# Performance work log

Measured on AMD Instinct MI355X. Metric: run time of the kernel, lower is better.

Reference implementation:

```python
import jax, jax.numpy as jnp
import numpy as np

N, S, F, D = 4096, 128, 128, 256  # batch, memory slots, feat_dim, dim_h_o
EPS = 1e-8  # torch CosineSimilarity eps


def _xavier(key, shape):
    fan_out, fan_in = shape
    std = float(np.sqrt(2.0 / (fan_in + fan_out)))
    return jax.random.normal(key, shape, dtype=jnp.float32) * std


def setup_inputs() -> dict:
    key = jax.random.key(0)
    ks = jax.random.split(key, 10)
    return {
        "h_o_prev": jax.random.normal(ks[0], (N, D), dtype=jnp.float32),
        "C": jax.random.normal(ks[1], (N, S, F), dtype=jnp.float32),
        "Wk": _xavier(ks[2], (F, D)), "bk": jnp.zeros((F,), jnp.float32),
        "Wb": _xavier(ks[3], (1, D)), "bb": jnp.zeros((1,), jnp.float32),
        "We": _xavier(ks[4], (F, D)), "be": jnp.zeros((F,), jnp.float32),
        "Wv": _xavier(ks[5], (F, D)), "bv": jnp.zeros((F,), jnp.float32),
        "Wih": _xavier(ks[6], (3 * D, F)), "Whh": _xavier(ks[7], (3 * D, D)),
        "bih": jnp.zeros((3 * D,), jnp.float32), "bhh": jnp.zeros((3 * D,), jnp.float32),
    }


def reference(h_o_prev, C, Wk, bk, Wb, bb, We, be, Wv, bv, Wih, Whh, bih, bhh):
    # --- Attention (content addressing) ---
    k = h_o_prev @ Wk.T + bk                              # [N, F]
    beta_pre = h_o_prev @ Wb.T + bb                       # [N, 1]
    # clamp-split softplus trick in source == softplus(x) + 1
    beta = jax.nn.softplus(beta_pre) + 1.0                # [N, 1]
    C_norm = jnp.maximum(jnp.linalg.norm(C, axis=2), EPS)           # [N, S]
    k_norm = jnp.maximum(jnp.linalg.norm(k, axis=1, keepdims=True), EPS)  # [N, 1]
    s = jnp.einsum("nsf,nf->ns", C, k) / (C_norm * k_norm)          # cosine sim [N, S]
    w = jax.nn.softmax(s * beta, axis=1)                  # [N, S]
    # --- Read memory ---
    r = jnp.einsum("ns,nsf->nf", w, C)                    # [N, F]
    # --- GRU cell update (torch GRUCell semantics) ---
    gi = r @ Wih.T + bih                                  # [N, 3D]
    gh = h_o_prev @ Whh.T + bhh                           # [N, 3D]
    i_r, i_z, i_n = jnp.split(gi, 3, axis=1)
    h_r, h_z, h_n = jnp.split(gh, 3, axis=1)
    rg = jax.nn.sigmoid(i_r + h_r)
    z = jax.nn.sigmoid(i_z + h_z)
    n = jnp.tanh(i_n + rg * h_n)
    h_o = (1.0 - z) * n + z * h_o_prev                    # [N, D]
    # --- Write memory (erase + add, outer products) ---
    e = jax.nn.sigmoid(h_o @ We.T + be)                   # [N, F]
    v = h_o @ Wv.T + bv                                   # [N, F]
    w2 = w[:, :, None]                                    # [N, S, 1]
    C_new = C * (1.0 - w2 * e[:, None, :]) + w2 * v[:, None, :]
    return h_o, C_new, k, r
```

## Files before the change

### kernel.cpp

```cpp
#include <hip/hip_runtime.h>
#include <hip/hip_bf16.h>
#include <cstddef>
#include <cstdint>

constexpr int Nn = 4096;
constexpr int Ss = 128;
constexpr int Ff = 128;
constexpr int Dd = 256;
constexpr float EPSV = 1e-8f;

constexpr size_t HO_OFF = 0;
constexpr size_t C_OFF  = (size_t)Nn * Dd;
constexpr size_t K_OFF  = C_OFF + (size_t)Nn * Ss * Ff;
constexpr size_t R_OFF  = K_OFF + (size_t)Nn * Ff;

typedef __attribute__((ext_vector_type(4))) float f4v;
typedef __attribute__((ext_vector_type(8))) short bh8;
typedef __attribute__((ext_vector_type(4))) short bh4;

constexpr int WK_O  = 0;
constexpr int WHH_O = 32768;
constexpr int WIH_O = 229376;
constexpr int WEV_O = 327680;
constexpr int W_TOT = 393216;

__device__ __forceinline__ float sigmf(float x) { return 1.0f / (1.0f + __expf(-x)); }

__device__ __forceinline__ short f2bf(float x) {
    __hip_bfloat16 h = __float2bfloat16(x);
    return *reinterpret_cast<short*>(&h);
}

__device__ __forceinline__ int swzH(int row, int kb) { return row * 512 + (kb ^ ((row & 7) << 4)); }
__device__ __forceinline__ int swzR(int row, int kb) { return row * 256 + (kb ^ ((row & 7) << 4)); }

__device__ __forceinline__ f4v mfma16(bh8 a, bh8 b, f4v c) {
    return __builtin_amdgcn_mfma_f32_16x16x32_bf16(a, b, c, 0, 0, 0);
}

__global__ __launch_bounds__(256) void prep_weights(
    const float* __restrict__ Wk, const float* __restrict__ Whh,
    const float* __restrict__ Wih, const float* __restrict__ We,
    const float* __restrict__ Wv, short* __restrict__ out)
{
    int id = blockIdx.x * 256 + threadIdx.x;
    float v;
    if      (id < WHH_O) v = Wk[id - WK_O];
    else if (id < WIH_O) v = Whh[id - WHH_O];
    else if (id < WEV_O) v = Wih[id - WIH_O];
    else if (id < WEV_O + 32768) v = We[id - WEV_O];
    else v = Wv[id - WEV_O - 32768];
    out[id] = f2bf(v);
}

__global__ __launch_bounds__(512, 4) void mega_kernel(
    const float* __restrict__ C, const float* __restrict__ h_prev,
    const short* __restrict__ WB,
    const float* __restrict__ Wb, const float* __restrict__ bb,
    const float* __restrict__ bk, const float* __restrict__ bhh,
    const float* __restrict__ bih, const float* __restrict__ be,
    const float* __restrict__ bv,
    float* __restrict__ ho, float* __restrict__ Cnew,
    float* __restrict__ kout, float* __restrict__ rout)
{
    __shared__ float sH[8][256];
    __shared__ __align__(16) short sHb[16 * 256];
    __shared__ __align__(16) short sRb[16 * 128];
    __shared__ float sK[8][128];
    __shared__ float sSc[8][128];
    __shared__ float sGs[8][768];
    __shared__ float sGn[8][256];
    __shared__ float sEV[8][256];

    const int t  = threadIdx.x;
    const int l  = t & 63;
    const int wv = t >> 6;
    const int nb = blockIdx.x * 8;
    char* hb = (char*)sHb;
    char* rb = (char*)sRb;

    const short* WkB  = WB + WK_O;
    const short* WhhB = WB + WHH_O;
    const short* WihB = WB + WIH_O;
    const short* WevB = WB + WEV_O;

    {
        const int f = t * 4, row = f >> 8, col = f & 255;
        float4 hv = *(const float4*)(h_prev + (size_t)(nb + row) * Dd + col);
        *(float4*)&sH[row][col] = hv;
        bh4 hb4 = { f2bf(hv.x), f2bf(hv.y), f2bf(hv.z), f2bf(hv.w) };
        *(bh4*)(hb + swzH(row, col * 2)) = hb4;
        *(int4*)(hb + 8192 + t * 16) = int4{0, 0, 0, 0};
        *(int*)(rb + 2048 + t * 4) = 0;
    }
    __syncthreads();

    {
        const int fr = l & 15, kq = l >> 4, rbase = kq * 4;
        const int colg = wv * 16 + fr;
        f4v acc = {0.f, 0.f, 0.f, 0.f};
#pragma unroll
        for (int kc = 0; kc < 8; ++kc) {
            bh8 a = *(const bh8*)(hb + swzH(fr, kc * 64 + kq * 16));
            bh8 b = *(const bh8*)(WkB + (size_t)colg * 256 + kc * 32 + kq * 8);
            acc = mfma16(a, b, acc);
        }
        if (rbase < 8) {
            const float bs = bk[colg];
#pragma unroll
            for (int rg = 0; rg < 4; ++rg) {
                float x = acc[rg] + bs;
                sK[rbase + rg][colg] = x;
                kout[(size_t)(nb + rbase + rg) * Ff + colg] = x;
            }
        }
    }
    __syncthreads();

    float M_r = 0.0f, invL_r = 0.0f;
    {
        const int half = l >> 5, fl = l & 31, f4 = fl * 4;
        const float* Cn = C + (size_t)(nb + wv) * (Ss * Ff);

        float kv0 = sK[wv][l], kv1 = sK[wv][64 + l];
        float ks = kv0 * kv0 + kv1 * kv1;
#pragma unroll
        for (int o = 32; o > 0; o >>= 1) ks += __shfl_xor(ks, o);
        const float knorm = fmaxf(sqrtf(ks), EPSV);

        float4 hv = *(const float4*)&sH[wv][l * 4];
        float4 wb4 = *(const float4*)(Wb + l * 4);
        float bp = hv.x * wb4.x + hv.y * wb4.y + hv.z * wb4.z + hv.w * wb4.w;
#pragma unroll
        for (int o = 32; o > 0; o >>= 1) bp += __shfl_xor(bp, o);
        bp += bb[0];
        const float beta = ((bp > 20.0f) ? bp : log1pf(__expf(bp))) + 1.0f;

        const float4 kreg = *(const float4*)&sK[wv][f4];
        float m = -INFINITY, lsum = 0.0f;
        f4v racc = {0.f, 0.f, 0.f, 0.f};
#pragma unroll 4
        for (int it = 0; it < 64; ++it) {
            const int s = it * 2 + half;
            f4v c4 = *(const f4v*)(Cn + s * Ff + f4);
            float d = c4.x * kreg.x + c4.y * kreg.y + c4.z * kreg.z + c4.w * kreg.w;
            float q = c4.x * c4.x + c4.y * c4.y + c4.z * c4.z + c4.w * c4.w;
#pragma unroll
            for (int o = 16; o > 0; o >>= 1) { d += __shfl_xor(d, o); q += __shfl_xor(q, o); }
            const float x = d / (fmaxf(sqrtf(q), EPSV) * knorm) * beta;
            if (fl == 0) sSc[wv][s] = x;
            const float mn   = fmaxf(m, x);
            const float corr = __expf(m - mn);
            const float p    = __expf(x - mn);
            lsum = lsum * corr + p;
            racc = racc * corr + p * c4;
            m = mn;
        }
        float m2 = __shfl_xor(m, 32);
        float l2 = __shfl_xor(lsum, 32);
        f4v r2;
        r2.x = __shfl_xor(racc.x, 32); r2.y = __shfl_xor(racc.y, 32);
        r2.z = __shfl_xor(racc.z, 32); r2.w = __shfl_xor(racc.w, 32);
        const float M  = fmaxf(m, m2);
        const float e1 = __expf(m - M), e2 = __expf(m2 - M);
        const float L  = lsum * e1 + l2 * e2;
        const float iL = 1.0f / L;
        f4v r4 = (racc * e1 + r2 * e2) * iL;
        if (half == 0) {
            *(f4v*)(rout + (size_t)(nb + wv) * Ff + f4) = r4;
            bh4 rb4 = { f2bf(r4.x), f2bf(r4.y), f2bf(r4.z), f2bf(r4.w) };
            *(bh4*)(rb + swzR(wv, f4 * 2)) = rb4;
        }
        M_r = M; invL_r = iL;
    }
    __syncthreads();

    {
        const int fr = l & 15, kq = l >> 4, rbase = kq * 4;
#pragma unroll
        for (int i = 0; i < 6; ++i) {
            const int colg = i * 128 + wv * 16 + fr;
            f4v aG = {0.f, 0.f, 0.f, 0.f}, aI = {0.f, 0.f, 0.f, 0.f};
#pragma unroll
            for (int kc = 0; kc < 8; ++kc) {
                bh8 a = *(const bh8*)(hb + swzH(fr, kc * 64 + kq * 16));
                bh8 b = *(const bh8*)(WhhB + (size_t)colg * 256 + kc * 32 + kq * 8);
                aG = mfma16(a, b, aG);
            }
#pragma unroll
            for (int kc = 0; kc < 4; ++kc) {
                bh8 a = *(const bh8*)(rb + swzR(fr, kc * 64 + kq * 16));
                bh8 b = *(const bh8*)(WihB + (size_t)colg * 128 + kc * 32 + kq * 8);
                aI = mfma16(a, b, aI);
            }
            if (rbase < 8) {
                if (colg < 512) {
                    const float bs = bhh[colg] + bih[colg];
#pragma unroll
                    for (int rg = 0; rg < 4; ++rg)
                        sGs[rbase + rg][colg] = aG[rg] + aI[rg] + bs;
                } else {
                    const float b1 = bhh[colg], b2 = bih[colg];
#pragma unroll
                    for (int rg = 0; rg < 4; ++rg) {
                        sGs[rbase + rg][colg]       = aG[rg] + b1;
                        sGn[rbase + rg][colg - 512] = aI[rg] + b2;
                    }
                }
            }
        }
    }
    __syncthreads();

    {
        const int d4 = l * 4;
        float4 gr  = *(const float4*)&sGs[wv][d4];
        float4 gz  = *(const float4*)&sGs[wv][256 + d4];
        float4 hn  = *(const float4*)&sGs[wv][512 + d4];
        float4 in_ = *(const float4*)&sGn[wv][d4];
        float4 hp  = *(const float4*)&sH[wv][d4];
        float4 o;
        { float rg = sigmf(gr.x), z = sigmf(gz.x);
          float nn = tanhf(in_.x + rg * hn.x); o.x = (1.0f - z) * nn + z * hp.x; }
        { float rg = sigmf(gr.y), z = sigmf(gz.y);
          float nn = tanhf(in_.y + rg * hn.y); o.y = (1.0f - z) * nn + z * hp.y; }
        { float rg = sigmf(gr.z), z = sigmf(gz.z);
          float nn = tanhf(in_.z + rg * hn.z); o.z = (1.0f - z) * nn + z * hp.z; }
        { float rg = sigmf(gr.w), z = sigmf(gz.w);
          float nn = tanhf(in_.w + rg * hn.w); o.w = (1.0f - z) * nn + z * hp.w; }
        *(float4*)(ho + (size_t)(nb + wv) * Dd + d4) = o;
        bh4 ob = { f2bf(o.x), f2bf(o.y), f2bf(o.z), f2bf(o.w) };
        *(bh4*)(hb + swzH(wv, d4 * 2)) = ob;
    }
    __syncthreads();

    {
        const int fr = l & 15, kq = l >> 4, rbase = kq * 4;
#pragma unroll
        for (int i = 0; i < 2; ++i) {
            const int colg = i * 128 + wv * 16 + fr;
            f4v acc = {0.f, 0.f, 0.f, 0.f};
#pragma unroll
            for (int kc = 0; kc < 8; ++kc) {
                bh8 a = *(const bh8*)(hb + swzH(fr, kc * 64 + kq * 16));
                bh8 b = *(const bh8*)(WevB + (size_t)colg * 256 + kc * 32 + kq * 8);
                acc = mfma16(a, b, acc);
            }
            if (rbase < 8) {
                const float bs = (colg < 128) ? be[colg] : bv[colg - 128];
#pragma unroll
                for (int rg = 0; rg < 4; ++rg) {
                    float x = acc[rg] + bs;
                    if (colg < 128) x = sigmf(x);
                    sEV[rbase + rg][colg] = x;
                }
            }
        }
    }
    __syncthreads();

    {
        const int half = l >> 5, fl = l & 31, f4 = fl * 4;
        const float* Cn = C    + (size_t)(nb + wv) * (Ss * Ff);
        float*       Co = Cnew + (size_t)(nb + wv) * (Ss * Ff);
        f4v e4 = *(const f4v*)&sEV[wv][f4];
        f4v v4 = *(const f4v*)&sEV[wv][128 + f4];
#pragma unroll 4
        for (int it = 0; it < 64; ++it) {
            const int s = it * 2 + half;
            const float wsc = __expf(sSc[wv][s] - M_r) * invL_r;
            f4v c4 = *(const f4v*)(Cn + s * Ff + f4);
            f4v o = c4 * (1.0f - wsc * e4) + wsc * v4;
            __builtin_nontemporal_store(o, (f4v*)(Co + s * Ff + f4));
        }
    }
}

extern "C" void kernel_launch(void* const* d_in, const int* in_sizes, int n_in,
                              void* d_out, int out_size, void* d_ws, size_t ws_size,
                              hipStream_t stream)
{
    const float* h_prev = (const float*)d_in[0];
    const float* C      = (const float*)d_in[1];
    const float* Wk     = (const float*)d_in[2];
    const float* bk     = (const float*)d_in[3];
    const float* Wb     = (const float*)d_in[4];
    const float* bb     = (const float*)d_in[5];
    const float* We     = (const float*)d_in[6];
    const float* be     = (const float*)d_in[7];
    const float* Wv     = (const float*)d_in[8];
    const float* bv     = (const float*)d_in[9];
    const float* Wih    = (const float*)d_in[10];
    const float* Whh    = (const float*)d_in[11];
    const float* bih    = (const float*)d_in[12];
    const float* bhh    = (const float*)d_in[13];

    float* out  = (float*)d_out;
    float* ho   = out + HO_OFF;
    float* Cnew = out + C_OFF;
    float* kbuf = out + K_OFF;
    float* rbuf = out + R_OFF;

    short* wsB = (short*)d_ws;

    prep_weights<<<W_TOT / 256, 256, 0, stream>>>(Wk, Whh, Wih, We, Wv, wsB);

    mega_kernel<<<Nn / 8, 512, 0, stream>>>(
        C, h_prev, wsB, Wb, bb, bk, bhh, bih, be, bv,
        ho, Cnew, kbuf, rbuf);
}
```

Before: 191.0 us.

## Prefetch C rows in register batches and use fixed-max softmax

Result: slower. 204.5 us (+7.1%).

```diff
diff --git a/kernel.cpp b/kernel.cpp
--- a/kernel.cpp
+++ b/kernel.cpp
@@ -117,7 +117,7 @@
     }
     __syncthreads();
 
-    float M_r = 0.0f, invL_r = 0.0f;
+    float invL_r = 0.0f;
     {
         const int half = l >> 5, fl = l & 31, f4 = fl * 4;
         const float* Cn = C + (size_t)(nb + wv) * (Ss * Ff);
@@ -137,41 +137,55 @@
         const float beta = ((bp > 20.0f) ? bp : log1pf(__expf(bp))) + 1.0f;
 
         const float4 kreg = *(const float4*)&sK[wv][f4];
-        float m = -INFINITY, lsum = 0.0f;
+        float lsum = 0.0f;
         f4v racc = {0.f, 0.f, 0.f, 0.f};
-#pragma unroll 4
-        for (int it = 0; it < 64; ++it) {
-            const int s = it * 2 + half;
-            f4v c4 = *(const f4v*)(Cn + s * Ff + f4);
-            float d = c4.x * kreg.x + c4.y * kreg.y + c4.z * kreg.z + c4.w * kreg.w;
-            float q = c4.x * c4.x + c4.y * c4.y + c4.z * c4.z + c4.w * c4.w;
-#pragma unroll
-            for (int o = 16; o > 0; o >>= 1) { d += __shfl_xor(d, o); q += __shfl_xor(q, o); }
-            const float x = d / (fmaxf(sqrtf(q), EPSV) * knorm) * beta;
-            if (fl == 0) sSc[wv][s] = x;
-            const float mn   = fmaxf(m, x);
-            const float corr = __expf(m - mn);
-            const float p    = __expf(x - mn);
-            lsum = lsum * corr + p;
-            racc = racc * corr + p * c4;
-            m = mn;
-        }
-        float m2 = __shfl_xor(m, 32);
-        float l2 = __shfl_xor(lsum, 32);
+
+        f4v buf[8];
+#pragma unroll
+        for (int j = 0; j < 8; ++j)
+            buf[j] = *(const f4v*)(Cn + (size_t)(j * 2 + half) * Ff + f4);
+        for (int g = 0; g < 8; ++g) {
+            f4v nxt[8];
+            if (g < 7) {
+#pragma unroll
+                for (int j = 0; j < 8; ++j)
+                    nxt[j] = *(const f4v*)(Cn + (size_t)((g + 1) * 16 + j * 2 + half) * Ff + f4);
+            }
+#pragma unroll
+            for (int j = 0; j < 8; ++j) {
+                const int s = g * 16 + j * 2 + half;
+                const f4v c4 = buf[j];
+                float d = c4.x * kreg.x + c4.y * kreg.y + c4.z * kreg.z + c4.w * kreg.w;
+                float q = c4.x * c4.x + c4.y * c4.y + c4.z * c4.z + c4.w * c4.w;
+#pragma unroll
+                for (int o = 16; o > 0; o >>= 1) {
+                    d += __shfl_xor(d, o);
+                    q += __shfl_xor(q, o);
+                }
+                const float cn = fmaxf(sqrtf(q), EPSV);
+                const float x = d / (cn * knorm) * beta;
+                const float p = __expf(x - beta);
+                if (fl == 0) sSc[wv][s] = p;
+                lsum += p;
+                racc += p * c4;
+            }
+            if (g < 7) {
+#pragma unroll
+                for (int j = 0; j < 8; ++j) buf[j] = nxt[j];
+            }
+        }
+        const float L = lsum + __shfl_xor(lsum, 32);
         f4v r2;
         r2.x = __shfl_xor(racc.x, 32); r2.y = __shfl_xor(racc.y, 32);
         r2.z = __shfl_xor(racc.z, 32); r2.w = __shfl_xor(racc.w, 32);
-        const float M  = fmaxf(m, m2);
-        const float e1 = __expf(m - M), e2 = __expf(m2 - M);
-        const float L  = lsum * e1 + l2 * e2;
         const float iL = 1.0f / L;
-        f4v r4 = (racc * e1 + r2 * e2) * iL;
+        f4v r4 = (racc + r2) * iL;
         if (half == 0) {
             *(f4v*)(rout + (size_t)(nb + wv) * Ff + f4) = r4;
             bh4 rb4 = { f2bf(r4.x), f2bf(r4.y), f2bf(r4.z), f2bf(r4.w) };
             *(bh4*)(rb + swzR(wv, f4 * 2)) = rb4;
         }
-        M_r = M; invL_r = iL;
+        invL_r = iL;
     }
     __syncthreads();
 
@@ -263,15 +277,32 @@
         const int half = l >> 5, fl = l & 31, f4 = fl * 4;
         const float* Cn = C    + (size_t)(nb + wv) * (Ss * Ff);
         float*       Co = Cnew + (size_t)(nb + wv) * (Ss * Ff);
-        f4v e4 = *(const f4v*)&sEV[wv][f4];
-        f4v v4 = *(const f4v*)&sEV[wv][128 + f4];
-#pragma unroll 4
-        for (int it = 0; it < 64; ++it) {
-            const int s = it * 2 + half;
-            const float wsc = __expf(sSc[wv][s] - M_r) * invL_r;
-            f4v c4 = *(const f4v*)(Cn + s * Ff + f4);
-            f4v o = c4 * (1.0f - wsc * e4) + wsc * v4;
-            __builtin_nontemporal_store(o, (f4v*)(Co + s * Ff + f4));
+        const f4v e4 = *(const f4v*)&sEV[wv][f4];
+        const f4v v4 = *(const f4v*)&sEV[wv][128 + f4];
+        const float iL = invL_r;
+
+        f4v buf[8];
+#pragma unroll
+        for (int j = 0; j < 8; ++j)
+            buf[j] = *(const f4v*)(Cn + (size_t)(j * 2 + half) * Ff + f4);
+        for (int g = 0; g < 8; ++g) {
+            f4v nxt[8];
+            if (g < 7) {
+#pragma unroll
+                for (int j = 0; j < 8; ++j)
+                    nxt[j] = *(const f4v*)(Cn + (size_t)((g + 1) * 16 + j * 2 + half) * Ff + f4);
+            }
+#pragma unroll
+            for (int j = 0; j < 8; ++j) {
+                const int s = g * 16 + j * 2 + half;
+                const float wsc = sSc[wv][s] * iL;
+                f4v o = buf[j] * (1.0f - wsc * e4) + wsc * v4;
+                __builtin_nontemporal_store(o, (f4v*)(Co + (size_t)s * Ff + f4));
+            }
+            if (g < 7) {
+#pragma unroll
+                for (int j = 0; j < 8; ++j) buf[j] = nxt[j];
+            }
         }
     }
 }
```
